# Performance work log

Hardware: AMD Instinct MI355X
Metric: run time of the kernel (lower is better)

## Reference

```python
import jax, jax.numpy as jnp
import numpy as np

NEG_SLOPE = 0.2
HEADS = 4
HEAD_DIM = 32


def setup_inputs() -> dict:
    key = jax.random.key(0)
    ks = jax.random.split(key, 6)
    N, E, D_IN = 50000, 600000, 128
    x = jax.random.normal(ks[0], (N, D_IN), dtype=jnp.float32)
    edge_index = jax.random.randint(ks[1], (2, E), 0, N, dtype=jnp.int64)
    W = jax.random.normal(ks[2], (D_IN, HEADS * HEAD_DIM), dtype=jnp.float32) * (1.0 / np.sqrt(D_IN))
    att_src = jax.random.normal(ks[3], (HEADS, HEAD_DIM), dtype=jnp.float32) * 0.1
    att_dst = jax.random.normal(ks[4], (HEADS, HEAD_DIM), dtype=jnp.float32) * 0.1
    bias = jax.random.normal(ks[5], (HEADS * HEAD_DIM,), dtype=jnp.float32) * 0.01
    return {"x": x, "edge_index": edge_index, "W": W, "att_src": att_src, "att_dst": att_dst, "bias": bias}


def reference(x, edge_index, W, att_src, att_dst, bias):
    N = x.shape[0]
    # add self-loops (PyG GATConv default add_self_loops=True)
    loop = jnp.arange(N, dtype=edge_index.dtype)
    src = jnp.concatenate([edge_index[0], loop])  # [E+N]
    dst = jnp.concatenate([edge_index[1], loop])
    # linear projection -> [N, H, D]
    h = (x @ W).reshape(N, HEADS, HEAD_DIM)
    # per-node attention halves: [N, H]
    a_src = jnp.einsum('nhd,hd->nh', h, att_src)
    a_dst = jnp.einsum('nhd,hd->nh', h, att_dst)
    # per-edge logits + leaky relu
    logits = a_src[src] + a_dst[dst]  # [E', H]
    logits = jnp.where(logits >= 0, logits, NEG_SLOPE * logits)
    # softmax over edges grouped by destination node
    m = jax.ops.segment_max(logits, dst, num_segments=N)  # [N, H]
    ealpha = jnp.exp(logits - m[dst])
    denom = jax.ops.segment_sum(ealpha, dst, num_segments=N)
    alpha = ealpha / denom[dst]  # every node has a self-loop -> denom > 0
    # weighted message aggregation: scatter-add h[src] * alpha -> dst
    msgs = h[src] * alpha[:, :, None]  # [E', H, D]
    out = jax.ops.segment_sum(msgs, dst, num_segments=N)  # [N, H, D]
    out = out.reshape(N, HEADS * HEAD_DIM) + bias
    return jnp.tanh(out)
```

## Files before the change

### kernel.cpp

```cpp
#include <hip/hip_runtime.h>
#include <hip/hip_bf16.h>
#include <math.h>

#define NEG_SLOPE 0.2f
#define DMODEL 128
#define CAP 96
#define POISON 0xAAAAAAAAu
#define DEGS 16

typedef __attribute__((ext_vector_type(8))) short short8;
typedef __attribute__((ext_vector_type(4))) float floatx4;

__device__ __forceinline__ float leaky(float x) { return x >= 0.f ? x : NEG_SLOPE * x; }
__device__ __forceinline__ float b2f(short v) {
    return __uint_as_float(((unsigned)(unsigned short)v) << 16);
}
__device__ __forceinline__ float fast_tanh(float x) {
    return 1.f - 2.f / (__expf(2.f * x) + 1.f);
}

__global__ __launch_bounds__(256) void kprep(
    const float* __restrict__ W, const float* __restrict__ att_src,
    const float* __restrict__ att_dst, __hip_bfloat16* __restrict__ Wt,
    __hip_bfloat16* __restrict__ Wat)
{
    int idx = blockIdx.x * 256 + threadIdx.x;
    if (idx < DMODEL * DMODEL) {
        int n = idx >> 7, k = idx & 127;
        Wt[idx] = __float2bfloat16(W[k * DMODEL + n]);
    }
    if (idx < 16 * DMODEL) {
        int col = idx >> 7, k = idx & 127;
        float v = 0.f;
        if (col < 8) {
            int hd = col & 3;
            const float* att = (col < 4) ? att_src : att_dst;
            #pragma unroll 8
            for (int d = 0; d < 32; d++)
                v += W[k * DMODEL + hd * 32 + d] * att[hd * 32 + d];
        }
        Wat[idx] = __float2bfloat16(v);
    }
}

__global__ __launch_bounds__(256) void kmerge(
    const float* __restrict__ x, const __hip_bfloat16* __restrict__ Wt,
    const __hip_bfloat16* __restrict__ Wat, const int* __restrict__ srcs,
    const int* __restrict__ dsts, __hip_bfloat16* __restrict__ h,
    float* __restrict__ a_src, float* __restrict__ a_dst,
    unsigned* __restrict__ deg, int* __restrict__ bucket,
    int E, int N, int nkcb)
{
    if ((int)blockIdx.x < nkcb) {
        int i = (blockIdx.x * 256 + threadIdx.x) * 8;
        if (i + 8 <= E) {
            int4 s0 = *(const int4*)(srcs + i);
            int4 s1 = *(const int4*)(srcs + i + 4);
            int4 d0 = *(const int4*)(dsts + i);
            int4 d1 = *(const int4*)(dsts + i + 4);
            int r0 = (int)(atomicAdd(&deg[(size_t)d0.x * DEGS], 1u) - POISON);
            int r1 = (int)(atomicAdd(&deg[(size_t)d0.y * DEGS], 1u) - POISON);
            int r2 = (int)(atomicAdd(&deg[(size_t)d0.z * DEGS], 1u) - POISON);
            int r3 = (int)(atomicAdd(&deg[(size_t)d0.w * DEGS], 1u) - POISON);
            int r4 = (int)(atomicAdd(&deg[(size_t)d1.x * DEGS], 1u) - POISON);
            int r5 = (int)(atomicAdd(&deg[(size_t)d1.y * DEGS], 1u) - POISON);
            int r6 = (int)(atomicAdd(&deg[(size_t)d1.z * DEGS], 1u) - POISON);
            int r7 = (int)(atomicAdd(&deg[(size_t)d1.w * DEGS], 1u) - POISON);
            bucket[(size_t)d0.x * CAP + r0] = s0.x;
            bucket[(size_t)d0.y * CAP + r1] = s0.y;
            bucket[(size_t)d0.z * CAP + r2] = s0.z;
            bucket[(size_t)d0.w * CAP + r3] = s0.w;
            bucket[(size_t)d1.x * CAP + r4] = s1.x;
            bucket[(size_t)d1.y * CAP + r5] = s1.y;
            bucket[(size_t)d1.z * CAP + r6] = s1.z;
            bucket[(size_t)d1.w * CAP + r7] = s1.w;
        } else if (i < E) {
            for (int e = i; e < E; e++) {
                int r = (int)(atomicAdd(&deg[(size_t)dsts[e] * DEGS], 1u) - POISON);
                bucket[(size_t)dsts[e] * CAP + r] = srcs[e];
            }
        }
        return;
    }
    const int wv = threadIdx.x >> 6, lane = threadIdx.x & 63;
    const int node0 = ((int)blockIdx.x - nkcb) * 64 + wv * 16;
    const int m = lane & 15, kq = lane >> 4;
    floatx4 acc[9];
    #pragma unroll
    for (int t = 0; t < 9; t++) acc[t] = (floatx4)(0.f);

    int arow = node0 + m; if (arow >= N) arow = N - 1;
    const float* ap = x + (size_t)arow * DMODEL + kq * 8;
    const short* bp = (const short*)Wt + m * DMODEL + kq * 8;
    const short* wp = (const short*)Wat + m * DMODEL + kq * 8;

    #pragma unroll
    for (int ks = 0; ks < 4; ks++) {
        float4 a0 = *(const float4*)(ap + ks * 32);
        float4 a1 = *(const float4*)(ap + ks * 32 + 4);
        __hip_bfloat16 ab[8] = {
            __float2bfloat16(a0.x), __float2bfloat16(a0.y),
            __float2bfloat16(a0.z), __float2bfloat16(a0.w),
            __float2bfloat16(a1.x), __float2bfloat16(a1.y),
            __float2bfloat16(a1.z), __float2bfloat16(a1.w)};
        short8 a = *(const short8*)ab;
        #pragma unroll
        for (int nt = 0; nt < 8; nt++) {
            short8 b = *(const short8*)(bp + nt * 16 * DMODEL + ks * 32);
            acc[nt] = __builtin_amdgcn_mfma_f32_16x16x32_bf16(a, b, acc[nt], 0, 0, 0);
        }
        short8 b8 = *(const short8*)(wp + ks * 32);
        acc[8] = __builtin_amdgcn_mfma_f32_16x16x32_bf16(a, b8, acc[8], 0, 0, 0);
    }

    #pragma unroll
    for (int nt = 0; nt < 8; nt++) {
        #pragma unroll
        for (int r = 0; r < 4; r++) {
            int node = node0 + kq * 4 + r;
            if (node < N)
                h[(size_t)node * DMODEL + nt * 16 + m] = __float2bfloat16(acc[nt][r]);
        }
    }
    if (m < 8) {
        #pragma unroll
        for (int r = 0; r < 4; r++) {
            int node = node0 + kq * 4 + r;
            if (node < N) {
                if (m < 4) a_src[(size_t)node * 4 + m] = acc[8][r];
                else       a_dst[(size_t)node * 4 + (m - 4)] = acc[8][r];
            }
        }
    }
}

__global__ __launch_bounds__(256) void kagg(
    const unsigned* __restrict__ deg, const int* __restrict__ bucket,
    const __hip_bfloat16* __restrict__ h, const float* __restrict__ a_src,
    const float* __restrict__ a_dst, const float* __restrict__ bias,
    float* __restrict__ out, int N)
{
    __shared__ float2 pid[8][32][4];
    const int hw = threadIdx.x >> 5;
    const int l = threadIdx.x & 31;
    const int head = l >> 3;
    const int node = blockIdx.x * 8 + hw;
    if (node >= N) return;

    const float4 adw = *(const float4*)(a_dst + (size_t)node * 4);
    const float4 asw = *(const float4*)(a_src + (size_t)node * 4);
    float4 ls;
    ls.x = leaky(asw.x + adw.x); ls.y = leaky(asw.y + adw.y);
    ls.z = leaky(asw.z + adw.z); ls.w = leaky(asw.w + adw.w);

    float4 denom4 = {0.f, 0.f, 0.f, 0.f};
    short4 hs = *(const short4*)(h + (size_t)node * DMODEL + l * 4);
    float4 acc = {b2f(hs.x), b2f(hs.y), b2f(hs.z), b2f(hs.w)};

    const int dcount = (int)(deg[(size_t)node * DEGS] - POISON);
    const int j0 = node * CAP, j1 = j0 + dcount;
    for (int base = j0; base < j1; base += 32) {
        int idx = base + l;
        bool valid = idx < j1;
        int sv = valid ? bucket[idx] : 0;
        float4 a4 = *(const float4*)(a_src + (size_t)sv * 4);
        float4 p4;
        p4.x = valid ? __expf(leaky(a4.x + adw.x) - ls.x) : 0.f;
        p4.y = valid ? __expf(leaky(a4.y + adw.y) - ls.y) : 0.f;
        p4.z = valid ? __expf(leaky(a4.z + adw.z) - ls.z) : 0.f;
        p4.w = valid ? __expf(leaky(a4.w + adw.w) - ls.w) : 0.f;
        denom4.x += p4.x; denom4.y += p4.y; denom4.z += p4.z; denom4.w += p4.w;
        float idf = __int_as_float(sv);
        float4 w0 = {p4.x, idf, p4.y, idf};
        float4 w1 = {p4.z, idf, p4.w, idf};
        *(float4*)&pid[hw][l][0] = w0;
        *(float4*)&pid[hw][l][2] = w1;
        int cnt = j1 - base; if (cnt > 32) cnt = 32;
        int rounded = (cnt + 7) & ~7;
        for (int jj = 0; jj < rounded; jj += 8) {
            float2 pi[8];
            #pragma unroll
            for (int q = 0; q < 8; q++) pi[q] = pid[hw][jj + q][head];
            short4 g[8];
            #pragma unroll
            for (int q = 0; q < 8; q++)
                g[q] = *(const short4*)(h + (size_t)__float_as_int(pi[q].y) * DMODEL + l * 4);
            #pragma unroll
            for (int q = 0; q < 8; q++) {
                acc.x += pi[q].x * b2f(g[q].x);
                acc.y += pi[q].x * b2f(g[q].y);
                acc.z += pi[q].x * b2f(g[q].z);
                acc.w += pi[q].x * b2f(g[q].w);
            }
        }
    }
    #pragma unroll
    for (int off = 1; off < 32; off <<= 1) {
        denom4.x += __shfl_xor(denom4.x, off, 64);
        denom4.y += __shfl_xor(denom4.y, off, 64);
        denom4.z += __shfl_xor(denom4.z, off, 64);
        denom4.w += __shfl_xor(denom4.w, off, 64);
    }
    float denom = 1.f + ((head == 0) ? denom4.x : (head == 1) ? denom4.y
                        : (head == 2) ? denom4.z : denom4.w);

    float4 b = *(const float4*)(bias + l * 4);
    float inv = 1.f / denom;
    float4 o;
    o.x = fast_tanh(acc.x * inv + b.x);
    o.y = fast_tanh(acc.y * inv + b.y);
    o.z = fast_tanh(acc.z * inv + b.z);
    o.w = fast_tanh(acc.w * inv + b.w);
    *(float4*)(out + (size_t)node * DMODEL + l * 4) = o;
}

extern "C" void kernel_launch(void* const* d_in, const int* in_sizes, int n_in,
                              void* d_out, int out_size, void* d_ws, size_t ws_size,
                              hipStream_t stream) {
    const float* x       = (const float*)d_in[0];
    const int*   edges   = (const int*)d_in[1];
    const float* W       = (const float*)d_in[2];
    const float* att_src = (const float*)d_in[3];
    const float* att_dst = (const float*)d_in[4];
    const float* bias    = (const float*)d_in[5];
    float* out = (float*)d_out;

    const int N = in_sizes[0] / DMODEL;
    const int E = in_sizes[1] / 2;
    const int* srcs = edges;
    const int* dsts = edges + E;

    __hip_bfloat16* Wt  = (__hip_bfloat16*)d_ws;
    __hip_bfloat16* Wat = Wt + DMODEL * DMODEL;
    __hip_bfloat16* h   = Wat + 16 * DMODEL;
    float* a_src_d = (float*)(h + (size_t)N * DMODEL);
    float* a_dst_d = a_src_d + (size_t)N * 4;
    unsigned* deg = (unsigned*)(a_dst_d + (size_t)N * 4);
    int* bucket   = (int*)(deg + (size_t)N * DEGS);

    const int nkcb = (E / 8 + 255) / 256;
    const int nmm  = (N + 63) / 64;

    kprep<<<65, 256, 0, stream>>>(W, att_src, att_dst, Wt, Wat);
    kmerge<<<nkcb + nmm, 256, 0, stream>>>(x, Wt, Wat, srcs, dsts, h,
                                           a_src_d, a_dst_d, deg, bucket,
                                           E, N, nkcb);
    kagg<<<(N + 7) / 8, 256, 0, stream>>>(deg, bucket, h, a_src_d, a_dst_d,
                                          bias, out, N);
}
```

Baseline: 159.2 us.

## Fuse prep, CSR build, projection and aggregation into one persistent kernel with grid barriers

Merges the three launches into a single persistent kernel of about 1024 blocks that runs three phases: weight prep, then CSR bucketing alongside the MFMA projection, then a grid-strided aggregation. Software grid barriers built on an atomic counter (relying on the poisoned workspace value) separate the phases. The goal is to remove launch gaps and inter-kernel drain. In exchange it adds barrier spin cost, cuts parallelism in the CSR and aggregation phases, and can deadlock if all blocks are not co-resident at once.

```diff
diff --git a/kernel.cpp b/kernel.cpp
--- a/kernel.cpp
+++ b/kernel.cpp
@@ -19,199 +19,213 @@
     return 1.f - 2.f / (__expf(2.f * x) + 1.f);
 }
 
-__global__ __launch_bounds__(256) void kprep(
-    const float* __restrict__ W, const float* __restrict__ att_src,
-    const float* __restrict__ att_dst, __hip_bfloat16* __restrict__ Wt,
-    __hip_bfloat16* __restrict__ Wat)
-{
-    int idx = blockIdx.x * 256 + threadIdx.x;
-    if (idx < DMODEL * DMODEL) {
-        int n = idx >> 7, k = idx & 127;
-        Wt[idx] = __float2bfloat16(W[k * DMODEL + n]);
-    }
-    if (idx < 16 * DMODEL) {
-        int col = idx >> 7, k = idx & 127;
-        float v = 0.f;
-        if (col < 8) {
-            int hd = col & 3;
-            const float* att = (col < 4) ? att_src : att_dst;
-            #pragma unroll 8
-            for (int d = 0; d < 32; d++)
-                v += W[k * DMODEL + hd * 32 + d] * att[hd * 32 + d];
-        }
-        Wat[idx] = __float2bfloat16(v);
-    }
-}
-
-__global__ __launch_bounds__(256) void kmerge(
-    const float* __restrict__ x, const __hip_bfloat16* __restrict__ Wt,
-    const __hip_bfloat16* __restrict__ Wat, const int* __restrict__ srcs,
-    const int* __restrict__ dsts, __hip_bfloat16* __restrict__ h,
+__device__ __forceinline__ void gridbar(unsigned* ctr, unsigned expect) {
+    __syncthreads();
+    if (threadIdx.x == 0) {
+        __threadfence();
+        __hip_atomic_fetch_add(ctr, 1u, __ATOMIC_RELAXED, __HIP_MEMORY_SCOPE_AGENT);
+        while ((unsigned)(__hip_atomic_load(ctr, __ATOMIC_RELAXED,
+                                            __HIP_MEMORY_SCOPE_AGENT) - POISON) < expect)
+            __builtin_amdgcn_s_sleep(2);
+        __threadfence();
+    }
+    __syncthreads();
+}
+
+__global__ __launch_bounds__(256, 4) void pgat(
+    const float* __restrict__ x, const float* __restrict__ W,
+    const float* __restrict__ att_src, const float* __restrict__ att_dst,
+    const float* __restrict__ bias, const int* __restrict__ srcs,
+    const int* __restrict__ dsts, __hip_bfloat16* __restrict__ Wt,
+    __hip_bfloat16* __restrict__ Wat, __hip_bfloat16* __restrict__ h,
     float* __restrict__ a_src, float* __restrict__ a_dst,
     unsigned* __restrict__ deg, int* __restrict__ bucket,
-    int E, int N, int nkcb)
-{
-    if ((int)blockIdx.x < nkcb) {
-        int i = (blockIdx.x * 256 + threadIdx.x) * 8;
-        if (i + 8 <= E) {
-            int4 s0 = *(const int4*)(srcs + i);
-            int4 s1 = *(const int4*)(srcs + i + 4);
-            int4 d0 = *(const int4*)(dsts + i);
-            int4 d1 = *(const int4*)(dsts + i + 4);
-            int r0 = (int)(atomicAdd(&deg[(size_t)d0.x * DEGS], 1u) - POISON);
-            int r1 = (int)(atomicAdd(&deg[(size_t)d0.y * DEGS], 1u) - POISON);
-            int r2 = (int)(atomicAdd(&deg[(size_t)d0.z * DEGS], 1u) - POISON);
-            int r3 = (int)(atomicAdd(&deg[(size_t)d0.w * DEGS], 1u) - POISON);
-            int r4 = (int)(atomicAdd(&deg[(size_t)d1.x * DEGS], 1u) - POISON);
-            int r5 = (int)(atomicAdd(&deg[(size_t)d1.y * DEGS], 1u) - POISON);
-            int r6 = (int)(atomicAdd(&deg[(size_t)d1.z * DEGS], 1u) - POISON);
-            int r7 = (int)(atomicAdd(&deg[(size_t)d1.w * DEGS], 1u) - POISON);
-            bucket[(size_t)d0.x * CAP + r0] = s0.x;
-            bucket[(size_t)d0.y * CAP + r1] = s0.y;
-            bucket[(size_t)d0.z * CAP + r2] = s0.z;
-            bucket[(size_t)d0.w * CAP + r3] = s0.w;
-            bucket[(size_t)d1.x * CAP + r4] = s1.x;
-            bucket[(size_t)d1.y * CAP + r5] = s1.y;
-            bucket[(size_t)d1.z * CAP + r6] = s1.z;
-            bucket[(size_t)d1.w * CAP + r7] = s1.w;
-        } else if (i < E) {
-            for (int e = i; e < E; e++) {
-                int r = (int)(atomicAdd(&deg[(size_t)dsts[e] * DEGS], 1u) - POISON);
-                bucket[(size_t)dsts[e] * CAP + r] = srcs[e];
-            }
-        }
-        return;
-    }
-    const int wv = threadIdx.x >> 6, lane = threadIdx.x & 63;
-    const int node0 = ((int)blockIdx.x - nkcb) * 64 + wv * 16;
-    const int m = lane & 15, kq = lane >> 4;
-    floatx4 acc[9];
-    #pragma unroll
-    for (int t = 0; t < 9; t++) acc[t] = (floatx4)(0.f);
-
-    int arow = node0 + m; if (arow >= N) arow = N - 1;
-    const float* ap = x + (size_t)arow * DMODEL + kq * 8;
-    const short* bp = (const short*)Wt + m * DMODEL + kq * 8;
-    const short* wp = (const short*)Wat + m * DMODEL + kq * 8;
-
-    #pragma unroll
-    for (int ks = 0; ks < 4; ks++) {
-        float4 a0 = *(const float4*)(ap + ks * 32);
-        float4 a1 = *(const float4*)(ap + ks * 32 + 4);
-        __hip_bfloat16 ab[8] = {
-            __float2bfloat16(a0.x), __float2bfloat16(a0.y),
-            __float2bfloat16(a0.z), __float2bfloat16(a0.w),
-            __float2bfloat16(a1.x), __float2bfloat16(a1.y),
-            __float2bfloat16(a1.z), __float2bfloat16(a1.w)};
-        short8 a = *(const short8*)ab;
-        #pragma unroll
-        for (int nt = 0; nt < 8; nt++) {
-            short8 b = *(const short8*)(bp + nt * 16 * DMODEL + ks * 32);
-            acc[nt] = __builtin_amdgcn_mfma_f32_16x16x32_bf16(a, b, acc[nt], 0, 0, 0);
-        }
-        short8 b8 = *(const short8*)(wp + ks * 32);
-        acc[8] = __builtin_amdgcn_mfma_f32_16x16x32_bf16(a, b8, acc[8], 0, 0, 0);
-    }
-
-    #pragma unroll
-    for (int nt = 0; nt < 8; nt++) {
-        #pragma unroll
-        for (int r = 0; r < 4; r++) {
-            int node = node0 + kq * 4 + r;
-            if (node < N)
-                h[(size_t)node * DMODEL + nt * 16 + m] = __float2bfloat16(acc[nt][r]);
-        }
-    }
-    if (m < 8) {
-        #pragma unroll
-        for (int r = 0; r < 4; r++) {
-            int node = node0 + kq * 4 + r;
-            if (node < N) {
-                if (m < 4) a_src[(size_t)node * 4 + m] = acc[8][r];
-                else       a_dst[(size_t)node * 4 + (m - 4)] = acc[8][r];
-            }
-        }
-    }
-}
-
-__global__ __launch_bounds__(256) void kagg(
-    const unsigned* __restrict__ deg, const int* __restrict__ bucket,
-    const __hip_bfloat16* __restrict__ h, const float* __restrict__ a_src,
-    const float* __restrict__ a_dst, const float* __restrict__ bias,
-    float* __restrict__ out, int N)
+    unsigned* __restrict__ bar, float* __restrict__ out,
+    int E, int N, int ncsr)
 {
     __shared__ float2 pid[8][32][4];
+    const unsigned grid = gridDim.x;
+
+    {
+        int idx = blockIdx.x * 256 + threadIdx.x;
+        if (idx < DMODEL * DMODEL) {
+            int n = idx >> 7, k = idx & 127;
+            Wt[idx] = __float2bfloat16(W[k * DMODEL + n]);
+        }
+        if (idx < 16 * DMODEL) {
+            int col = idx >> 7, k = idx & 127;
+            float v = 0.f;
+            if (col < 8) {
+                int hd = col & 3;
+                const float* att = (col < 4) ? att_src : att_dst;
+                #pragma unroll 8
+                for (int d = 0; d < 32; d++)
+                    v += W[k * DMODEL + hd * 32 + d] * att[hd * 32 + d];
+            }
+            Wat[idx] = __float2bfloat16(v);
+        }
+    }
+    gridbar(bar, grid);
+
+    if ((int)blockIdx.x < ncsr) {
+        const int stride8 = ncsr * 256 * 8;
+        for (int i = (blockIdx.x * 256 + threadIdx.x) * 8; i < E; i += stride8) {
+            if (i + 8 <= E) {
+                int4 s0 = *(const int4*)(srcs + i);
+                int4 s1 = *(const int4*)(srcs + i + 4);
+                int4 d0 = *(const int4*)(dsts + i);
+                int4 d1 = *(const int4*)(dsts + i + 4);
+                int r0 = (int)(atomicAdd(&deg[(size_t)d0.x * DEGS], 1u) - POISON);
+                int r1 = (int)(atomicAdd(&deg[(size_t)d0.y * DEGS], 1u) - POISON);
+                int r2 = (int)(atomicAdd(&deg[(size_t)d0.z * DEGS], 1u) - POISON);
+                int r3 = (int)(atomicAdd(&deg[(size_t)d0.w * DEGS], 1u) - POISON);
+                int r4 = (int)(atomicAdd(&deg[(size_t)d1.x * DEGS], 1u) - POISON);
+                int r5 = (int)(atomicAdd(&deg[(size_t)d1.y * DEGS], 1u) - POISON);
+                int r6 = (int)(atomicAdd(&deg[(size_t)d1.z * DEGS], 1u) - POISON);
+                int r7 = (int)(atomicAdd(&deg[(size_t)d1.w * DEGS], 1u) - POISON);
+                bucket[(size_t)d0.x * CAP + r0] = s0.x;
+                bucket[(size_t)d0.y * CAP + r1] = s0.y;
+                bucket[(size_t)d0.z * CAP + r2] = s0.z;
+                bucket[(size_t)d0.w * CAP + r3] = s0.w;
+                bucket[(size_t)d1.x * CAP + r4] = s1.x;
+                bucket[(size_t)d1.y * CAP + r5] = s1.y;
+                bucket[(size_t)d1.z * CAP + r6] = s1.z;
+                bucket[(size_t)d1.w * CAP + r7] = s1.w;
+            } else {
+                for (int e = i; e < E; e++) {
+                    int r = (int)(atomicAdd(&deg[(size_t)dsts[e] * DEGS], 1u) - POISON);
+                    bucket[(size_t)dsts[e] * CAP + r] = srcs[e];
+                }
+            }
+        }
+    } else {
+        const int wv = threadIdx.x >> 6, lane = threadIdx.x & 63;
+        const int node0 = ((int)blockIdx.x - ncsr) * 64 + wv * 16;
+        const int m = lane & 15, kq = lane >> 4;
+        floatx4 acc[9];
+        #pragma unroll
+        for (int t = 0; t < 9; t++) acc[t] = (floatx4)(0.f);
+
+        int arow = node0 + m; if (arow >= N) arow = N - 1;
+        const float* ap = x + (size_t)arow * DMODEL + kq * 8;
+        const short* bp = (const short*)Wt + m * DMODEL + kq * 8;
+        const short* wp = (const short*)Wat + m * DMODEL + kq * 8;
+
+        #pragma unroll
+        for (int ks = 0; ks < 4; ks++) {
+            float4 a0 = *(const float4*)(ap + ks * 32);
+            float4 a1 = *(const float4*)(ap + ks * 32 + 4);
+            __hip_bfloat16 ab[8] = {
+                __float2bfloat16(a0.x), __float2bfloat16(a0.y),
+                __float2bfloat16(a0.z), __float2bfloat16(a0.w),
+                __float2bfloat16(a1.x), __float2bfloat16(a1.y),
+                __float2bfloat16(a1.z), __float2bfloat16(a1.w)};
+            short8 a = *(const short8*)ab;
+            #pragma unroll
+            for (int nt = 0; nt < 8; nt++) {
+                short8 b = *(const short8*)(bp + nt * 16 * DMODEL + ks * 32);
+                acc[nt] = __builtin_amdgcn_mfma_f32_16x16x32_bf16(a, b, acc[nt], 0, 0, 0);
+            }
+            short8 b8 = *(const short8*)(wp + ks * 32);
+            acc[8] = __builtin_amdgcn_mfma_f32_16x16x32_bf16(a, b8, acc[8], 0, 0, 0);
+        }
+
+        #pragma unroll
+        for (int nt = 0; nt < 8; nt++) {
+            #pragma unroll
+            for (int r = 0; r < 4; r++) {
+                int node = node0 + kq * 4 + r;
+                if (node < N)
+                    h[(size_t)node * DMODEL + nt * 16 + m] = __float2bfloat16(acc[nt][r]);
+            }
+        }
+        if (m < 8) {
+            #pragma unroll
+            for (int r = 0; r < 4; r++) {
+                int node = node0 + kq * 4 + r;
+                if (node < N) {
+                    if (m < 4) a_src[(size_t)node * 4 + m] = acc[8][r];
+                    else       a_dst[(size_t)node * 4 + (m - 4)] = acc[8][r];
+                }
+            }
+        }
+    }
+    gridbar(bar + 16, grid);
+
     const int hw = threadIdx.x >> 5;
     const int l = threadIdx.x & 31;
     const int head = l >> 3;
-    const int node = blockIdx.x * 8 + hw;
-    if (node >= N) return;
-
-    const float4 adw = *(const float4*)(a_dst + (size_t)node * 4);
-    const float4 asw = *(const float4*)(a_src + (size_t)node * 4);
-    float4 ls;
-    ls.x = leaky(asw.x + adw.x); ls.y = leaky(asw.y + adw.y);
-    ls.z = leaky(asw.z + adw.z); ls.w = leaky(asw.w + adw.w);
-
-    float4 denom4 = {0.f, 0.f, 0.f, 0.f};
-    short4 hs = *(const short4*)(h + (size_t)node * DMODEL + l * 4);
-    float4 acc = {b2f(hs.x), b2f(hs.y), b2f(hs.z), b2f(hs.w)};
-
-    const int dcount = (int)(deg[(size_t)node * DEGS] - POISON);
-    const int j0 = node * CAP, j1 = j0 + dcount;
-    for (int base = j0; base < j1; base += 32) {
-        int idx = base + l;
-        bool valid = idx < j1;
-        int sv = valid ? bucket[idx] : 0;
-        float4 a4 = *(const float4*)(a_src + (size_t)sv * 4);
-        float4 p4;
-        p4.x = valid ? __expf(leaky(a4.x + adw.x) - ls.x) : 0.f;
-        p4.y = valid ? __expf(leaky(a4.y + adw.y) - ls.y) : 0.f;
-        p4.z = valid ? __expf(leaky(a4.z + adw.z) - ls.z) : 0.f;
-        p4.w = valid ? __expf(leaky(a4.w + adw.w) - ls.w) : 0.f;
-        denom4.x += p4.x; denom4.y += p4.y; denom4.z += p4.z; denom4.w += p4.w;
-        float idf = __int_as_float(sv);
-        float4 w0 = {p4.x, idf, p4.y, idf};
-        float4 w1 = {p4.z, idf, p4.w, idf};
-        *(float4*)&pid[hw][l][0] = w0;
-        *(float4*)&pid[hw][l][2] = w1;
-        int cnt = j1 - base; if (cnt > 32) cnt = 32;
-        int rounded = (cnt + 7) & ~7;
-        for (int jj = 0; jj < rounded; jj += 8) {
-            float2 pi[8];
-            #pragma unroll
-            for (int q = 0; q < 8; q++) pi[q] = pid[hw][jj + q][head];
-            short4 g[8];
-            #pragma unroll
-            for (int q = 0; q < 8; q++)
-                g[q] = *(const short4*)(h + (size_t)__float_as_int(pi[q].y) * DMODEL + l * 4);
-            #pragma unroll
-            for (int q = 0; q < 8; q++) {
-                acc.x += pi[q].x * b2f(g[q].x);
-                acc.y += pi[q].x * b2f(g[q].y);
-                acc.z += pi[q].x * b2f(g[q].z);
-                acc.w += pi[q].x * b2f(g[q].w);
-            }
-        }
-    }
-    #pragma unroll
-    for (int off = 1; off < 32; off <<= 1) {
-        denom4.x += __shfl_xor(denom4.x, off, 64);
-        denom4.y += __shfl_xor(denom4.y, off, 64);
-        denom4.z += __shfl_xor(denom4.z, off, 64);
-        denom4.w += __shfl_xor(denom4.w, off, 64);
-    }
-    float denom = 1.f + ((head == 0) ? denom4.x : (head == 1) ? denom4.y
-                        : (head == 2) ? denom4.z : denom4.w);
-
-    float4 b = *(const float4*)(bias + l * 4);
-    float inv = 1.f / denom;
-    float4 o;
-    o.x = fast_tanh(acc.x * inv + b.x);
-    o.y = fast_tanh(acc.y * inv + b.y);
-    o.z = fast_tanh(acc.z * inv + b.z);
-    o.w = fast_tanh(acc.w * inv + b.w);
-    *(float4*)(out + (size_t)node * DMODEL + l * 4) = o;
+    const int nbmax = (N + 7) / 8;
+    for (int nb = blockIdx.x; nb < nbmax; nb += grid) {
+        const int node = nb * 8 + hw;
+        if (node >= N) continue;
+
+        const float4 adw = *(const float4*)(a_dst + (size_t)node * 4);
+        const float4 asw = *(const float4*)(a_src + (size_t)node * 4);
+        float4 ls;
+        ls.x = leaky(asw.x + adw.x); ls.y = leaky(asw.y + adw.y);
+        ls.z = leaky(asw.z + adw.z); ls.w = leaky(asw.w + adw.w);
+
+        float4 denom4 = {0.f, 0.f, 0.f, 0.f};
+        short4 hs = *(const short4*)(h + (size_t)node * DMODEL + l * 4);
+        float4 acc = {b2f(hs.x), b2f(hs.y), b2f(hs.z), b2f(hs.w)};
+
+        const int dcount = (int)(deg[(size_t)node * DEGS] - POISON);
+        const int j0 = node * CAP, j1 = j0 + dcount;
+        for (int base = j0; base < j1; base += 32) {
+            int idx = base + l;
+            bool valid = idx < j1;
+            int sv = valid ? bucket[idx] : 0;
+            float4 a4 = *(const float4*)(a_src + (size_t)sv * 4);
+            float4 p4;
+            p4.x = valid ? __expf(leaky(a4.x + adw.x) - ls.x) : 0.f;
+            p4.y = valid ? __expf(leaky(a4.y + adw.y) - ls.y) : 0.f;
+            p4.z = valid ? __expf(leaky(a4.z + adw.z) - ls.z) : 0.f;
+            p4.w = valid ? __expf(leaky(a4.w + adw.w) - ls.w) : 0.f;
+            denom4.x += p4.x; denom4.y += p4.y; denom4.z += p4.z; denom4.w += p4.w;
+            float idf = __int_as_float(sv);
+            float4 w0 = {p4.x, idf, p4.y, idf};
+            float4 w1 = {p4.z, idf, p4.w, idf};
+            *(float4*)&pid[hw][l][0] = w0;
+            *(float4*)&pid[hw][l][2] = w1;
+            int cnt = j1 - base; if (cnt > 32) cnt = 32;
+            int rounded = (cnt + 7) & ~7;
+            for (int jj = 0; jj < rounded; jj += 8) {
+                float2 pi[8];
+                #pragma unroll
+                for (int q = 0; q < 8; q++) pi[q] = pid[hw][jj + q][head];
+                short4 g[8];
+                #pragma unroll
+                for (int q = 0; q < 8; q++)
+                    g[q] = *(const short4*)(h + (size_t)__float_as_int(pi[q].y) * DMODEL + l * 4);
+                #pragma unroll
+                for (int q = 0; q < 8; q++) {
+                    acc.x += pi[q].x * b2f(g[q].x);
+                    acc.y += pi[q].x * b2f(g[q].y);
+                    acc.z += pi[q].x * b2f(g[q].z);
+                    acc.w += pi[q].x * b2f(g[q].w);
+                }
+            }
+        }
+        #pragma unroll
+        for (int off = 1; off < 32; off <<= 1) {
+            denom4.x += __shfl_xor(denom4.x, off, 64);
+            denom4.y += __shfl_xor(denom4.y, off, 64);
+            denom4.z += __shfl_xor(denom4.z, off, 64);
+            denom4.w += __shfl_xor(denom4.w, off, 64);
+        }
+        float denom = 1.f + ((head == 0) ? denom4.x : (head == 1) ? denom4.y
+                            : (head == 2) ? denom4.z : denom4.w);
+
+        float4 b = *(const float4*)(bias + l * 4);
+        float inv = 1.f / denom;
+        float4 o;
+        o.x = fast_tanh(acc.x * inv + b.x);
+        o.y = fast_tanh(acc.y * inv + b.y);
+        o.z = fast_tanh(acc.z * inv + b.z);
+        o.w = fast_tanh(acc.w * inv + b.w);
+        *(float4*)(out + (size_t)node * DMODEL + l * 4) = o;
+    }
 }
 
 extern "C" void kernel_launch(void* const* d_in, const int* in_sizes, int n_in,
@@ -237,14 +251,14 @@
     float* a_dst_d = a_src_d + (size_t)N * 4;
     unsigned* deg = (unsigned*)(a_dst_d + (size_t)N * 4);
     int* bucket   = (int*)(deg + (size_t)N * DEGS);
-
-    const int nkcb = (E / 8 + 255) / 256;
-    const int nmm  = (N + 63) / 64;
-
-    kprep<<<65, 256, 0, stream>>>(W, att_src, att_dst, Wt, Wat);
-    kmerge<<<nkcb + nmm, 256, 0, stream>>>(x, Wt, Wat, srcs, dsts, h,
-                                           a_src_d, a_dst_d, deg, bucket,
-                                           E, N, nkcb);
-    kagg<<<(N + 7) / 8, 256, 0, stream>>>(deg, bucket, h, a_src_d, a_dst_d,
-                                          bias, out, N);
-}
+    unsigned* bar = (unsigned*)(bucket + (size_t)N * CAP);
+
+    int nmm  = (N + 63) / 64;
+    int ncsr = 1024 - nmm;
+    if (ncsr < 32) ncsr = 32;
+
+    pgat<<<ncsr + nmm, 256, 0, stream>>>(x, W, att_src, att_dst, bias,
+                                         srcs, dsts, Wt, Wat, h,
+                                         a_src_d, a_dst_d, deg, bucket, bar,
+                                         out, E, N, ncsr);
+}
```

Result: slower. 379.1 us (+138.1%).
